# Kernel optimization log

Hardware: AMD Instinct MI355X
Metric: run time of the kernel (lower is better)

## Reference

```python
import jax, jax.numpy as jnp
from jax import lax
import numpy as np
import math

EPS = 1e-5
LEVELS = 17  # quantized levels round(x*255/16) for x in [0,1) -> 0..16


def _bn(x, g, b):
    # training-mode BatchNorm2d: batch statistics over (B,H,W), biased var
    m = x.mean(axis=(0, 2, 3), keepdims=True)
    v = x.var(axis=(0, 2, 3), keepdims=True)
    return (x - m) / jnp.sqrt(v + EPS) * g[None, :, None, None] + b[None, :, None, None]


def _mode_pool_11(x):
    # x is pre-quantized to k*16/256, k in 0..16 -> sliding-window mode via per-level counts
    q = jnp.round(x * 16.0).astype(jnp.int32)  # recover integer level k
    qp = jnp.pad(q, ((0, 0), (0, 0), (5, 5), (5, 5)), mode='reflect')
    oh = (qp[:, :, None, :, :] == jnp.arange(LEVELS, dtype=jnp.int32)[None, None, :, None, None]).astype(jnp.float32)  # [B,C,L,H+10,W+10]
    counts = lax.reduce_window(oh, 0.0, lax.add, (1, 1, 1, 11, 11), (1, 1, 1, 1, 1), 'VALID')  # [B,C,L,H,W]
    lvl = jnp.argmax(counts, axis=2)  # ties -> smallest level, matching torch.mode
    return lvl.astype(x.dtype) * (16.0 / 256.0)


def setup_inputs() -> dict:
    key = jax.random.key(0)
    ks = jax.random.split(key, 8)
    B, C, H, W, F = 2, 3, 512, 512, 16
    x = jax.random.uniform(ks[0], (B, C, H, W), jnp.float32)
    w1 = jax.random.normal(ks[1], (F, C), jnp.float32) * 0.1
    b1 = jnp.zeros((F,), jnp.float32)
    g1 = jnp.ones((F,), jnp.float32); be1 = jnp.zeros((F,), jnp.float32)
    w2 = jax.random.normal(ks[2], (F, F), jnp.float32) * 0.1
    b2 = jnp.zeros((F,), jnp.float32)
    g2 = jnp.ones((F,), jnp.float32); be2 = jnp.zeros((F,), jnp.float32)
    dw = jax.random.normal(ks[3], (F, 1, 3, 3), jnp.float32) * 0.1  # depthwise 3x3
    gd = jnp.ones((F,), jnp.float32); bd = jnp.zeros((F,), jnp.float32)
    ww = jax.random.normal(ks[4], (F,), jnp.float32) * 0.1  # depthwise 1x1 = per-channel scale
    gw = jnp.ones((F,), jnp.float32); bw = jnp.zeros((F,), jnp.float32)
    wh = jax.random.normal(ks[5], (F,), jnp.float32) * 0.1
    gh = jnp.ones((F,), jnp.float32); bh = jnp.zeros((F,), jnp.float32)
    return dict(x=x, w1=w1, b1=b1, g1=g1, be1=be1, w2=w2, b2=b2, g2=g2, be2=be2,
                dw=dw, gd=gd, bd=bd, ww=ww, gw=gw, bw=bw, wh=wh, gh=gh, bh=bh)


def reference(x, w1, b1, g1, be1, w2, b2, g2, be2, dw, gd, bd, ww, gw, bw, wh, gh, bh):
    lrelu = jax.nn.leaky_relu  # default slope 0.01 matches torch LeakyReLU
    x = jnp.round(x * 255.0 / 16.0) * 16.0 / 256.0  # quantize to 16-ish levels
    x = _mode_pool_11(x)
    B, C, H, W = x.shape
    F = w1.shape[0]
    # prepare: two 1x1 conv + BN + LeakyReLU blocks
    p = jnp.einsum('oc,bchw->bohw', w1, x) + b1[None, :, None, None]
    p = lrelu(_bn(p, g1, be1))
    p = jnp.einsum('oc,bchw->bohw', w2, p) + b2[None, :, None, None]
    p = lrelu(_bn(p, g2, be2))
    inter = jnp.stack([p, p], axis=0).reshape(B, 2 * F, H, W)  # mirrors torch stack(dim=0).reshape
    d = p
    n = math.floor(math.log(min(H, W), 3))
    for _ in range(n):
        d = lax.conv_general_dilated(d, dw, (1, 1), 'SAME', feature_group_count=F,
                                     dimension_numbers=('NCHW', 'OIHW', 'NCHW'))
        d = lrelu(_bn(d, gd, bd))
        wdt = lrelu(_bn(d * ww[None, :, None, None], gw, bw))
        hgt = lrelu(_bn(d * wh[None, :, None, None], gh, bh))
        sc = jnp.stack([wdt, hgt], axis=1).reshape(B, 2 * F, H, W)
        inter = sc + inter
    return inter
```

## Files before the change

### kernel.cpp

```cpp
#include <hip/hip_runtime.h>
#include <hip/hip_bf16.h>
#include <stdint.h>
#include <stddef.h>

#define HW 262144
#define EPSF 1e-5f

typedef __hip_bfloat16 bf16;

__device__ __forceinline__ float us2f(uint32_t u){
  union { uint32_t i; float f; } c; c.i = u << 16; return c.f;
}
__device__ __forceinline__ ushort f2bu(float v){
  union { bf16 h; ushort u; } c; c.h = __float2bfloat16(v); return c.u;
}
__device__ __forceinline__ float lrelu(float v){ return v > 0.0f ? v : 0.01f * v; }
__device__ __forceinline__ uint32_t umax2(uint32_t a, uint32_t b){ return a > b ? a : b; }

__global__ __launch_bounds__(256) void k_quant_pad(const float* __restrict__ x,
                                                   uint8_t* __restrict__ qpad){
  int idx = blockIdx.x * 256 + threadIdx.x;
  if (idx >= 6 * 522 * 522) return;
  int pw = idx % 522; int t = idx / 522; int ph = t % 522; int img = t / 522;
  int h = ph - 5; h = h < 0 ? -h : h; if (h > 511) h = 1022 - h;
  int w = pw - 5; w = w < 0 ? -w : w; if (w > 511) w = 1022 - w;
  float v = x[img * HW + h * 512 + w];
  int k = (int)rintf((v * 255.0f) / 16.0f);
  qpad[img * (522 * 528) + ph * 528 + pw] = (uint8_t)k;
}

__global__ __launch_bounds__(256) void k_mode(const uint8_t* __restrict__ qpad,
                                              uint8_t* __restrict__ xm){
  __shared__ uint8_t tile[14 * 528];
  int tid = threadIdx.x;
  int img = blockIdx.x >> 7;
  int h0  = (blockIdx.x & 127) << 2;
  {
    const uint4* g4 = (const uint4*)(qpad + img * (522 * 528) + h0 * 528);
    uint4* t4 = (uint4*)tile;
    t4[tid] = g4[tid];
    if (tid < 206) t4[tid + 256] = g4[tid + 256];
  }
  __syncthreads();
  int r4 = tid >> 6;
  int w0 = (tid & 63) << 3;
  const uint8_t* base = tile + r4 * 528 + w0;
  uint32_t c0 = 0, c1 = 0, c2 = 0, c3 = 0, c4 = 0;
#define HINC(q) { uint32_t inc_ = 1u << (((q) & 3u) << 3); uint32_t rr_ = (q) >> 2; \
    c0 += (rr_==0u)?inc_:0u; c1 += (rr_==1u)?inc_:0u; c2 += (rr_==2u)?inc_:0u; \
    c3 += (rr_==3u)?inc_:0u; c4 += (rr_==4u)?inc_:0u; }
#define HDEC(q) { uint32_t inc_ = 1u << (((q) & 3u) << 3); uint32_t rr_ = (q) >> 2; \
    c0 -= (rr_==0u)?inc_:0u; c1 -= (rr_==1u)?inc_:0u; c2 -= (rr_==2u)?inc_:0u; \
    c3 -= (rr_==3u)?inc_:0u; c4 -= (rr_==4u)?inc_:0u; }
  #pragma unroll 1
  for (int r = 0; r < 11; ++r){
    const uint8_t* row = base + r * 528;
    #pragma unroll
    for (int j = 0; j < 11; ++j){ uint32_t q = row[j]; HINC(q); }
  }
  uint64_t packed = 0;
  #pragma unroll 1
  for (int s = 0; s < 8; ++s){
#define KEY(reg, sh, l) (((((reg) >> (sh)) & 0xffu) << 5) | (16u - (uint32_t)(l)))
    uint32_t m0 = umax2(umax2(KEY(c0,0,0),  KEY(c0,8,1)),  umax2(KEY(c0,16,2),  KEY(c0,24,3)));
    uint32_t m1 = umax2(umax2(KEY(c1,0,4),  KEY(c1,8,5)),  umax2(KEY(c1,16,6),  KEY(c1,24,7)));
    uint32_t m2 = umax2(umax2(KEY(c2,0,8),  KEY(c2,8,9)),  umax2(KEY(c2,16,10), KEY(c2,24,11)));
    uint32_t m3 = umax2(umax2(KEY(c3,0,12), KEY(c3,8,13)), umax2(KEY(c3,16,14), KEY(c3,24,15)));
    uint32_t m  = umax2(umax2(umax2(m0, m1), umax2(m2, m3)), KEY(c4,0,16));
#undef KEY
    uint32_t lvl = 16u - (m & 31u);
    packed |= ((uint64_t)lvl) << (8 * s);
    if (s < 7){
      #pragma unroll
      for (int r = 0; r < 11; ++r){
        uint32_t qo = base[r * 528 + s];      HDEC(qo);
        uint32_t qn = base[r * 528 + s + 11]; HINC(qn);
      }
    }
  }
#undef HINC
#undef HDEC
  *(uint64_t*)(xm + img * HW + (h0 + r4) * 512 + w0) = packed;
}

__device__ __forceinline__ void reduce16(float* su, float* sq, float* __restrict__ partials){
  __shared__ float lsum[32];
  int tid = threadIdx.x;
  if (tid < 32) lsum[tid] = 0.0f;
  __syncthreads();
  #pragma unroll
  for (int o = 0; o < 16; ++o){
    float s = su[o], q = sq[o];
    #pragma unroll
    for (int off = 32; off >= 1; off >>= 1){
      s += __shfl_xor(s, off);
      q += __shfl_xor(q, off);
    }
    if ((tid & 63) == 0){ atomicAdd(&lsum[o], s); atomicAdd(&lsum[16 + o], q); }
  }
  __syncthreads();
  if (tid < 32) partials[blockIdx.x * 32 + tid] = lsum[tid];
}

__global__ __launch_bounds__(256) void k_stats1(const uint8_t* __restrict__ xm,
                                                const float* __restrict__ w1,
                                                const float* __restrict__ b1,
                                                float* __restrict__ partials){
  int t0 = (blockIdx.x * 256 + threadIdx.x) << 2;
  int b = t0 >> 18, hw = t0 & (HW - 1);
  uint32_t q0 = *(const uint32_t*)(xm + (b * 3 + 0) * HW + hw);
  uint32_t q1 = *(const uint32_t*)(xm + (b * 3 + 1) * HW + hw);
  uint32_t q2 = *(const uint32_t*)(xm + (b * 3 + 2) * HW + hw);
  float su[16], sq[16];
  #pragma unroll
  for (int o = 0; o < 16; ++o){ su[o] = 0.0f; sq[o] = 0.0f; }
  #pragma unroll
  for (int px = 0; px < 4; ++px){
    float x0 = (float)((q0 >> (8 * px)) & 0xffu) * 0.0625f;
    float x1 = (float)((q1 >> (8 * px)) & 0xffu) * 0.0625f;
    float x2 = (float)((q2 >> (8 * px)) & 0xffu) * 0.0625f;
    #pragma unroll
    for (int o = 0; o < 16; ++o){
      float v = b1[o] + w1[o*3]*x0 + w1[o*3+1]*x1 + w1[o*3+2]*x2;
      su[o] += v; sq[o] += v * v;
    }
  }
  reduce16(su, sq, partials);
}

__global__ __launch_bounds__(256) void k_stats2(const uint8_t* __restrict__ xm,
                                                const float* __restrict__ w1,
                                                const float* __restrict__ b1,
                                                const float* __restrict__ w2,
                                                const float* __restrict__ b2,
                                                const float* __restrict__ params,
                                                float* __restrict__ partials){
  int t0 = (blockIdx.x * 256 + threadIdx.x) << 2;
  int b = t0 >> 18, hw = t0 & (HW - 1);
  uint32_t q0 = *(const uint32_t*)(xm + (b * 3 + 0) * HW + hw);
  uint32_t q1 = *(const uint32_t*)(xm + (b * 3 + 1) * HW + hw);
  uint32_t q2 = *(const uint32_t*)(xm + (b * 3 + 2) * HW + hw);
  float tv[4][16];
  #pragma unroll
  for (int px = 0; px < 4; ++px){
    float x0 = (float)((q0 >> (8 * px)) & 0xffu) * 0.0625f;
    float x1 = (float)((q1 >> (8 * px)) & 0xffu) * 0.0625f;
    float x2 = (float)((q2 >> (8 * px)) & 0xffu) * 0.0625f;
    #pragma unroll
    for (int o = 0; o < 16; ++o){
      float v = b1[o] + w1[o*3]*x0 + w1[o*3+1]*x1 + w1[o*3+2]*x2;
      tv[px][o] = lrelu(v * params[o] + params[16 + o]);
    }
  }
  float su[16], sq[16];
  #pragma unroll
  for (int o = 0; o < 16; ++o){ su[o] = 0.0f; sq[o] = 0.0f; }
  #pragma unroll
  for (int o = 0; o < 16; ++o){
    #pragma unroll
    for (int px = 0; px < 4; ++px){
      float acc = b2[o];
      #pragma unroll
      for (int c = 0; c < 16; ++c) acc = fmaf(w2[o*16 + c], tv[px][c], acc);
      su[o] += acc; sq[o] += acc * acc;
    }
  }
  reduce16(su, sq, partials);
}

__global__ __launch_bounds__(256) void k_prep(const uint8_t* __restrict__ xm,
                                              const float* __restrict__ w1,
                                              const float* __restrict__ b1,
                                              const float* __restrict__ w2,
                                              const float* __restrict__ b2,
                                              const float* __restrict__ params,
                                              bf16* __restrict__ p){
  int t0 = (blockIdx.x * 256 + threadIdx.x) << 2;
  int b = t0 >> 18, hw = t0 & (HW - 1);
  uint32_t q0 = *(const uint32_t*)(xm + (b * 3 + 0) * HW + hw);
  uint32_t q1 = *(const uint32_t*)(xm + (b * 3 + 1) * HW + hw);
  uint32_t q2 = *(const uint32_t*)(xm + (b * 3 + 2) * HW + hw);
  float tv[4][16];
  #pragma unroll
  for (int px = 0; px < 4; ++px){
    float x0 = (float)((q0 >> (8 * px)) & 0xffu) * 0.0625f;
    float x1 = (float)((q1 >> (8 * px)) & 0xffu) * 0.0625f;
    float x2 = (float)((q2 >> (8 * px)) & 0xffu) * 0.0625f;
    #pragma unroll
    for (int o = 0; o < 16; ++o){
      float v = b1[o] + w1[o*3]*x0 + w1[o*3+1]*x1 + w1[o*3+2]*x2;
      tv[px][o] = lrelu(v * params[o] + params[16 + o]);
    }
  }
  #pragma unroll
  for (int o = 0; o < 16; ++o){
    uint32_t w01 = 0, w23 = 0;
    #pragma unroll
    for (int px = 0; px < 4; ++px){
      float acc = b2[o];
      #pragma unroll
      for (int c = 0; c < 16; ++c) acc = fmaf(w2[o*16 + c], tv[px][c], acc);
      float v = lrelu(acc * params[32 + o] + params[48 + o]);
      uint32_t bits = (uint32_t)f2bu(v);
      if (px == 0) w01 = bits;
      else if (px == 1) w01 |= bits << 16;
      else if (px == 2) w23 = bits;
      else w23 |= bits << 16;
    }
    uint2 ov; ov.x = w01; ov.y = w23;
    *(uint2*)((ushort*)p + (b * 16 + o) * HW + hw) = ov;
  }
}

__device__ __forceinline__ void load_row10(const ushort* __restrict__ rp, int w0, float* v){
  uint4 cc = *(const uint4*)(rp + w0);
  uint32_t l = (w0 == 0)   ? 0u : (uint32_t)rp[w0 - 1];
  uint32_t r = (w0 == 504) ? 0u : (uint32_t)rp[w0 + 8];
  v[0] = us2f(l);
  v[1] = us2f(cc.x & 0xffffu); v[2] = us2f(cc.x >> 16);
  v[3] = us2f(cc.y & 0xffffu); v[4] = us2f(cc.y >> 16);
  v[5] = us2f(cc.z & 0xffffu); v[6] = us2f(cc.z >> 16);
  v[7] = us2f(cc.w & 0xffffu); v[8] = us2f(cc.w >> 16);
  v[9] = us2f(r);
}

__device__ __forceinline__ void zero_row10(float* v){
  #pragma unroll
  for (int j = 0; j < 10; ++j) v[j] = 0.0f;
}

__device__ __forceinline__ void reduce2(float s, float q, float* __restrict__ partials){
  __shared__ float l2[2];
  int tid = threadIdx.x;
  if (tid < 2) l2[tid] = 0.0f;
  __syncthreads();
  #pragma unroll
  for (int off = 32; off >= 1; off >>= 1){
    s += __shfl_xor(s, off);
    q += __shfl_xor(q, off);
  }
  if ((tid & 63) == 0){ atomicAdd(&l2[0], s); atomicAdd(&l2[1], q); }
  __syncthreads();
  if (tid < 2) partials[blockIdx.x * 2 + tid] = l2[tid];
}

__global__ __launch_bounds__(256) void k_convstat(const bf16* __restrict__ d,
                                                  const float* __restrict__ dw,
                                                  float* __restrict__ P1,
                                                  bf16* __restrict__ cout){
  int bid = blockIdx.x;
  int plane = bid >> 7, rg = bid & 127;
  int f = plane & 15;
  int tid = threadIdx.x;
  int h  = (rg << 2) + (tid >> 6);
  int w0 = (tid & 63) << 3;
  const ushort* pl = (const ushort*)d + plane * HW;
  float wf[9];
  #pragma unroll
  for (int i = 0; i < 9; ++i) wf[i] = dw[f * 9 + i];
  float v[3][10];
  #pragma unroll
  for (int dy = 0; dy < 3; ++dy){
    int row = h + dy - 1;
    if ((unsigned)row < 512u) load_row10(pl + row * 512, w0, v[dy]);
    else zero_row10(v[dy]);
  }
  float s = 0.0f, q = 0.0f;
  uint32_t cb[4];
  #pragma unroll
  for (int k = 0; k < 8; ++k){
    float acc = 0.0f;
    #pragma unroll
    for (int dy = 0; dy < 3; ++dy)
      #pragma unroll
      for (int dx = 0; dx < 3; ++dx)
        acc = fmaf(wf[dy*3 + dx], v[dy][k + dx], acc);
    s += acc; q += acc * acc;
    uint32_t bits = (uint32_t)f2bu(acc);
    if ((k & 1) == 0) cb[k >> 1] = bits; else cb[k >> 1] |= bits << 16;
  }
  uint4 cv; cv.x = cb[0]; cv.y = cb[1]; cv.z = cb[2]; cv.w = cb[3];
  *(uint4*)((ushort*)cout + plane * HW + h * 512 + w0) = cv;
  reduce2(s, q, P1);
}

__device__ __forceinline__ void chan_sum_wave(const float* __restrict__ P, int f, int lane,
                                              double& S, double& Q){
  S = 0.0; Q = 0.0;
  #pragma unroll
  for (int i = 0; i < 4; ++i){
    int e = lane + i * 64;
    int blk = (((e >> 7) * 16 + f) << 7) + (e & 127);
    S += (double)P[blk * 2];
    Q += (double)P[blk * 2 + 1];
  }
  #pragma unroll
  for (int off = 32; off >= 1; off >>= 1){
    S += __shfl_xor(S, off);
    Q += __shfl_xor(Q, off);
  }
}

__global__ __launch_bounds__(256) void k_bnfused(const bf16* __restrict__ cin,
                                                 const float* __restrict__ dw,
                                                 const float* __restrict__ gd,
                                                 const float* __restrict__ bd,
                                                 const float* __restrict__ P1in,
                                                 bf16* __restrict__ dout,
                                                 bf16* __restrict__ cout,
                                                 float* __restrict__ P2out,
                                                 float* __restrict__ P1out,
                                                 int write_c){
  __shared__ ushort strip[6][512];
  __shared__ float acc4[4];
  int bid = blockIdx.x;
  int plane = bid >> 7, rg = bid & 127;
  int f = plane & 15;
  int tid = threadIdx.x;

  double S, Q;
  chan_sum_wave(P1in, f, tid & 63, S, Q);
  float sc, sh;
  {
    double m = S / 524288.0;
    double v = Q / 524288.0 - m * m;
    sc = gd[f] / sqrtf((float)v + EPSF);
    sh = bd[f] - (float)m * sc;
  }
  if (tid < 4) acc4[tid] = 0.0f;

  int h0 = rg << 2;
  int h  = h0 + (tid >> 6);
  int w0 = (tid & 63) << 3;
  const ushort* cpl = (const ushort*)cin + plane * HW;

  float s2 = 0.0f, q2 = 0.0f;
  {
    uint4 cv = *(const uint4*)(cpl + h * 512 + w0);
    float cf[8];
    cf[0] = us2f(cv.x & 0xffffu); cf[1] = us2f(cv.x >> 16);
    cf[2] = us2f(cv.y & 0xffffu); cf[3] = us2f(cv.y >> 16);
    cf[4] = us2f(cv.z & 0xffffu); cf[5] = us2f(cv.z >> 16);
    cf[6] = us2f(cv.w & 0xffffu); cf[7] = us2f(cv.w >> 16);
    uint32_t ob[4];
    #pragma unroll
    for (int k = 0; k < 8; ++k){
      float vv = lrelu(fmaf(cf[k], sc, sh));
      uint32_t bits = (uint32_t)f2bu(vv);
      if ((k & 1) == 0) ob[k >> 1] = bits; else ob[k >> 1] |= bits << 16;
      s2 += vv; q2 += vv * vv;
    }
    uint4 ov; ov.x = ob[0]; ov.y = ob[1]; ov.z = ob[2]; ov.w = ob[3];
    *(uint4*)((ushort*)dout + plane * HW + h * 512 + w0) = ov;
    *(uint4*)&strip[1 + (tid >> 6)][w0] = ov;
  }

  if (tid < 128){
    int hh = (tid < 64) ? (h0 - 1) : (h0 + 4);
    int si = (tid < 64) ? 0 : 5;
    int wh0 = (tid & 63) << 3;
    uint4 hv; hv.x = 0; hv.y = 0; hv.z = 0; hv.w = 0;
    if ((unsigned)hh < 512u){
      uint4 cv = *(const uint4*)(cpl + hh * 512 + wh0);
      float cf[8];
      cf[0] = us2f(cv.x & 0xffffu); cf[1] = us2f(cv.x >> 16);
      cf[2] = us2f(cv.y & 0xffffu); cf[3] = us2f(cv.y >> 16);
      cf[4] = us2f(cv.z & 0xffffu); cf[5] = us2f(cv.z >> 16);
      cf[6] = us2f(cv.w & 0xffffu); cf[7] = us2f(cv.w >> 16);
      uint32_t hb[4];
      #pragma unroll
      for (int k = 0; k < 8; ++k){
        float vv = lrelu(fmaf(cf[k], sc, sh));
        uint32_t bits = (uint32_t)f2bu(vv);
        if ((k & 1) == 0) hb[k >> 1] = bits; else hb[k >> 1] |= bits << 16;
      }
      hv.x = hb[0]; hv.y = hb[1]; hv.z = hb[2]; hv.w = hb[3];
    }
    *(uint4*)&strip[si][wh0] = hv;
  }
  __syncthreads();

  float wf[9];
  #pragma unroll
  for (int i = 0; i < 9; ++i) wf[i] = dw[f * 9 + i];
  float s1 = 0.0f, q1 = 0.0f;
  {
    int si = 1 + (tid >> 6);
    float v[3][10];
    #pragma unroll
    for (int dy = 0; dy < 3; ++dy)
      load_row10(&strip[si - 1 + dy][0], w0, v[dy]);
    uint32_t cb[4];
    #pragma unroll
    for (int k = 0; k < 8; ++k){
      float acc = 0.0f;
      #pragma unroll
      for (int dy = 0; dy < 3; ++dy)
        #pragma unroll
        for (int dx = 0; dx < 3; ++dx)
          acc = fmaf(wf[dy*3 + dx], v[dy][k + dx], acc);
      s1 += acc; q1 += acc * acc;
      uint32_t bits = (uint32_t)f2bu(acc);
      if ((k & 1) == 0) cb[k >> 1] = bits; else cb[k >> 1] |= bits << 16;
    }
    if (write_c){
      uint4 cv2; cv2.x = cb[0]; cv2.y = cb[1]; cv2.z = cb[2]; cv2.w = cb[3];
      *(uint4*)((ushort*)cout + plane * HW + h * 512 + w0) = cv2;
    }
  }

  #pragma unroll
  for (int off = 32; off >= 1; off >>= 1){
    s2 += __shfl_xor(s2, off);
    q2 += __shfl_xor(q2, off);
    s1 += __shfl_xor(s1, off);
    q1 += __shfl_xor(q1, off);
  }
  if ((tid & 63) == 0){
    atomicAdd(&acc4[0], s2); atomicAdd(&acc4[1], q2);
    atomicAdd(&acc4[2], s1); atomicAdd(&acc4[3], q1);
  }
  __syncthreads();
  if (tid < 2)      P2out[bid * 2 + tid]       = acc4[tid];
  else if (tid < 4) P1out[bid * 2 + (tid - 2)] = acc4[tid];
}

__global__ __launch_bounds__(256) void k_fin_prep(const float* __restrict__ partials,
                                                  const float* __restrict__ g,
                                                  const float* __restrict__ bb,
                                                  float* __restrict__ params,
                                                  int offS, int offT){
  int tid = threadIdx.x;
  int o = tid & 15, c = tid >> 4;
  double S = 0.0, Q = 0.0;
  for (int i = c * 32; i < (c + 1) * 32; ++i){
    S += (double)partials[i * 32 + o];
    Q += (double)partials[i * 32 + 16 + o];
  }
  __shared__ double lS[256], lQ[256];
  lS[tid] = S; lQ[tid] = Q; __syncthreads();
  for (int st = 8; st >= 1; st >>= 1){
    if (c < st){ lS[tid] += lS[tid + st * 16]; lQ[tid] += lQ[tid + st * 16]; }
    __syncthreads();
  }
  if (tid < 16){
    double m = lS[tid] / 524288.0;
    double v = lQ[tid] / 524288.0 - m * m;
    float sc = g[tid] / sqrtf((float)v + EPSF);
    params[offS + tid] = sc;
    params[offT + tid] = bb[tid] - (float)m * sc;
  }
}

__global__ __launch_bounds__(256) void k_fin_all(const float* __restrict__ P2,
                                                 const float* __restrict__ ww,
                                                 const float* __restrict__ gw,
                                                 const float* __restrict__ bw,
                                                 const float* __restrict__ wh,
                                                 const float* __restrict__ gh,
                                                 const float* __restrict__ bh,
                                                 float* __restrict__ dparams){
  int tid = threadIdx.x;
  int wid = tid >> 6, lane = tid & 63;
  int pair = blockIdx.x * 4 + wid;
  int t = pair >> 4, f = pair & 15;
  double S, Q;
  chan_sum_wave(P2 + t * 8192, f, lane, S, Q);
  if (lane == 0){
    float m = (float)(S / 524288.0);
    float v = (float)(Q / 524288.0) - m * m;
    float sw = ww[f] * gw[f] / sqrtf(ww[f] * ww[f] * v + EPSF);
    float tw = bw[f] - m * sw;
    float s2 = wh[f] * gh[f] / sqrtf(wh[f] * wh[f] * v + EPSF);
    float t2 = bh[f] - m * s2;
    dparams[t * 64 + f]      = sw;
    dparams[t * 64 + 16 + f] = tw;
    dparams[t * 64 + 32 + f] = s2;
    dparams[t * 64 + 48 + f] = t2;
  }
}

__device__ __forceinline__ void conv8(uint4 cc, float* v){
  v[0] = us2f(cc.x & 0xffffu); v[1] = us2f(cc.x >> 16);
  v[2] = us2f(cc.y & 0xffffu); v[3] = us2f(cc.y >> 16);
  v[4] = us2f(cc.z & 0xffffu); v[5] = us2f(cc.z >> 16);
  v[6] = us2f(cc.w & 0xffffu); v[7] = us2f(cc.w >> 16);
}

__global__ __launch_bounds__(256) void k_final(const bf16* __restrict__ p,
                                               const bf16* __restrict__ d1,
                                               const bf16* __restrict__ d2,
                                               const bf16* __restrict__ d3,
                                               const bf16* __restrict__ d4,
                                               const bf16* __restrict__ d5,
                                               const float* __restrict__ dparams,
                                               float* __restrict__ out){
  int tid = threadIdx.x;
  int f = blockIdx.x >> 7;
  int gid = blockIdx.x * 256 + tid;
  int hw = (gid & 32767) << 3;
  int fo = f * HW + hw;
  int f1 = (16 + f) * HW + hw;

  uint4 rp0 = *(const uint4*)((const ushort*)p + fo);
  uint4 rp1 = *(const uint4*)((const ushort*)p + f1);
  uint4 r0a = *(const uint4*)((const ushort*)d1 + fo);
  uint4 r0b = *(const uint4*)((const ushort*)d1 + f1);
  uint4 r1a = *(const uint4*)((const ushort*)d2 + fo);
  uint4 r1b = *(const uint4*)((const ushort*)d2 + f1);
  uint4 r2a = *(const uint4*)((const ushort*)d3 + fo);
  uint4 r2b = *(const uint4*)((const ushort*)d3 + f1);
  uint4 r3a = *(const uint4*)((const ushort*)d4 + fo);
  uint4 r3b = *(const uint4*)((const ushort*)d4 + f1);
  uint4 r4a = *(const uint4*)((const ushort*)d5 + fo);
  uint4 r4b = *(const uint4*)((const ushort*)d5 + f1);

  float swA[5], twA[5], shA[5], thA[5];
  #pragma unroll
  for (int t = 0; t < 5; ++t){
    swA[t] = dparams[t * 64 + f];
    twA[t] = dparams[t * 64 + 16 + f];
    shA[t] = dparams[t * 64 + 32 + f];
    thA[t] = dparams[t * 64 + 48 + f];
  }

  float pf[8], pg[8];
  conv8(rp0, pf); conv8(rp1, pg);
  float a00[8], a01[8], a10[8], a11[8];
  #pragma unroll
  for (int k = 0; k < 8; ++k){ a00[k] = pf[k]; a01[k] = pg[k]; a10[k] = pf[k]; a11[k] = pg[k]; }

  uint4 ra[5] = { r0a, r1a, r2a, r3a, r4a };
  uint4 rb[5] = { r0b, r1b, r2b, r3b, r4b };
  #pragma unroll
  for (int t = 0; t < 5; ++t){
    float dv0[8], dv1[8];
    conv8(ra[t], dv0); conv8(rb[t], dv1);
    float sw = swA[t], tw = twA[t], sh = shA[t], th = thA[t];
    #pragma unroll
    for (int k = 0; k < 8; ++k){
      a00[k] += lrelu(fmaf(dv0[k], sw, tw));
      a01[k] += lrelu(fmaf(dv0[k], sh, th));
      a10[k] += lrelu(fmaf(dv1[k], sw, tw));
      a11[k] += lrelu(fmaf(dv1[k], sh, th));
    }
  }
  #pragma unroll
  for (int half = 0; half < 2; ++half){
    float4 v0 = { a00[half*4+0], a00[half*4+1], a00[half*4+2], a00[half*4+3] };
    float4 v1 = { a01[half*4+0], a01[half*4+1], a01[half*4+2], a01[half*4+3] };
    float4 v2 = { a10[half*4+0], a10[half*4+1], a10[half*4+2], a10[half*4+3] };
    float4 v3 = { a11[half*4+0], a11[half*4+1], a11[half*4+2], a11[half*4+3] };
    *(float4*)(out + f * HW + hw + half*4)        = v0;
    *(float4*)(out + (16 + f) * HW + hw + half*4) = v1;
    *(float4*)(out + (32 + f) * HW + hw + half*4) = v2;
    *(float4*)(out + (48 + f) * HW + hw + half*4) = v3;
  }
}

extern "C" void kernel_launch(void* const* d_in, const int* in_sizes, int n_in,
                              void* d_out, int out_size, void* d_ws, size_t ws_size,
                              hipStream_t stream){
  (void)in_sizes; (void)n_in; (void)out_size;
  const float* x   = (const float*)d_in[0];
  const float* w1  = (const float*)d_in[1];
  const float* b1  = (const float*)d_in[2];
  const float* g1  = (const float*)d_in[3];
  const float* be1 = (const float*)d_in[4];
  const float* w2  = (const float*)d_in[5];
  const float* b2  = (const float*)d_in[6];
  const float* g2  = (const float*)d_in[7];
  const float* be2 = (const float*)d_in[8];
  const float* dw  = (const float*)d_in[9];
  const float* gd  = (const float*)d_in[10];
  const float* bd  = (const float*)d_in[11];
  const float* ww  = (const float*)d_in[12];
  const float* gw  = (const float*)d_in[13];
  const float* bw  = (const float*)d_in[14];
  const float* wh  = (const float*)d_in[15];
  const float* gh  = (const float*)d_in[16];
  const float* bh  = (const float*)d_in[17];
  float* out = (float*)d_out;

  char* ws = (char*)d_ws;
  size_t off = 0;
  auto alloc = [&](size_t sz) -> void* {
    void* ptr = ws + off;
    off = (off + sz + 4095) & ~(size_t)4095;
    return ptr;
  };
  uint8_t* qpad  = (uint8_t*)alloc((size_t)6 * 522 * 528);
  uint8_t* xm    = (uint8_t*)alloc((size_t)6 * HW);
  bf16*    p     = (bf16*)   alloc((size_t)32 * HW * 2);
  bf16*    dbuf[5];
  for (int i = 0; i < 5; ++i) dbuf[i] = (bf16*)alloc((size_t)32 * HW * 2);
  float*   Pp     = (float*)  alloc((size_t)512 * 32 * 4);
  float*   P1a    = (float*)  alloc((size_t)4096 * 2 * 4);
  float*   P1b    = (float*)  alloc((size_t)4096 * 2 * 4);
  float*   P2     = (float*)  alloc((size_t)5 * 4096 * 2 * 4);
  float*   params = (float*)  alloc(4096);
  float*   dparams= (float*)  alloc(4096);
  if (ws_size < off) return;

  bf16* cbuf_a = (bf16*)(out + 8 * 1024 * 1024);
  bf16* cbuf_b = cbuf_a + (size_t)32 * HW;

  k_quant_pad<<<dim3((6*522*522 + 255)/256), dim3(256), 0, stream>>>(x, qpad);
  k_mode     <<<dim3(768), dim3(256), 0, stream>>>(qpad, xm);
  k_stats1   <<<dim3(512), dim3(256), 0, stream>>>(xm, w1, b1, Pp);
  k_fin_prep <<<dim3(1),   dim3(256), 0, stream>>>(Pp, g1, be1, params, 0, 16);
  k_stats2   <<<dim3(512), dim3(256), 0, stream>>>(xm, w1, b1, w2, b2, params, Pp);
  k_fin_prep <<<dim3(1),   dim3(256), 0, stream>>>(Pp, g2, be2, params, 32, 48);
  k_prep     <<<dim3(512), dim3(256), 0, stream>>>(xm, w1, b1, w2, b2, params, p);
  k_convstat <<<dim3(4096), dim3(256), 0, stream>>>(p, dw, P1a, cbuf_a);

  bf16* cin = cbuf_a; bf16* cout = cbuf_b;
  float* Pin = P1a; float* Pout = P1b;
  for (int t = 0; t < 5; ++t){
    k_bnfused<<<dim3(4096), dim3(256), 0, stream>>>(cin, dw, gd, bd, Pin,
                                                    dbuf[t], cout, P2 + t * 8192,
                                                    Pout, (t < 4) ? 1 : 0);
    bf16* ctmp = cin; cin = cout; cout = ctmp;
    float* tmp = Pin; Pin = Pout; Pout = tmp;
  }
  k_fin_all<<<dim3(20), dim3(256), 0, stream>>>(P2, ww, gw, bw, wh, gh, bh, dparams);
  k_final<<<dim3(2048), dim3(256), 0, stream>>>(p, dbuf[0], dbuf[1], dbuf[2],
                                                dbuf[3], dbuf[4], dparams, out);
}
```

Measured before the change: 223.6 us.

## Fuse conv loop, stats finalize and output into one persistent kernel with grid barriers

Replaces the separate convstat, five bnfused launches, fin_all and final kernels with a single 1024-block persistent kernel. Device-wide atomic-counter barriers separate the iterations, and each block now processes 16 rows instead of 4. The aim is to remove roughly eight kernel launches and their gaps, and to cut halo re-reads. It depends on all 1024 blocks being co-resident, which launch_bounds(256,4) is meant to allow on the device's CUs. If they are not co-resident the barrier can deadlock, and each barrier adds spin-wait cost.

```diff
diff --git a/kernel.cpp b/kernel.cpp
--- a/kernel.cpp
+++ b/kernel.cpp
@@ -5,6 +5,7 @@
 
 #define HW 262144
 #define EPSF 1e-5f
+#define NBLK 1024
 
 typedef __hip_bfloat16 bf16;
 
@@ -174,7 +175,9 @@
                                               const float* __restrict__ w2,
                                               const float* __restrict__ b2,
                                               const float* __restrict__ params,
-                                              bf16* __restrict__ p){
+                                              bf16* __restrict__ p,
+                                              unsigned* __restrict__ barcnt){
+  if (blockIdx.x == 0 && threadIdx.x == 0) *barcnt = 0u;
   int t0 = (blockIdx.x * 256 + threadIdx.x) << 2;
   int b = t0 >> 18, hw = t0 & (HW - 1);
   uint32_t q0 = *(const uint32_t*)(xm + (b * 3 + 0) * HW + hw);
@@ -210,219 +213,6 @@
     uint2 ov; ov.x = w01; ov.y = w23;
     *(uint2*)((ushort*)p + (b * 16 + o) * HW + hw) = ov;
   }
-}
-
-__device__ __forceinline__ void load_row10(const ushort* __restrict__ rp, int w0, float* v){
-  uint4 cc = *(const uint4*)(rp + w0);
-  uint32_t l = (w0 == 0)   ? 0u : (uint32_t)rp[w0 - 1];
-  uint32_t r = (w0 == 504) ? 0u : (uint32_t)rp[w0 + 8];
-  v[0] = us2f(l);
-  v[1] = us2f(cc.x & 0xffffu); v[2] = us2f(cc.x >> 16);
-  v[3] = us2f(cc.y & 0xffffu); v[4] = us2f(cc.y >> 16);
-  v[5] = us2f(cc.z & 0xffffu); v[6] = us2f(cc.z >> 16);
-  v[7] = us2f(cc.w & 0xffffu); v[8] = us2f(cc.w >> 16);
-  v[9] = us2f(r);
-}
-
-__device__ __forceinline__ void zero_row10(float* v){
-  #pragma unroll
-  for (int j = 0; j < 10; ++j) v[j] = 0.0f;
-}
-
-__device__ __forceinline__ void reduce2(float s, float q, float* __restrict__ partials){
-  __shared__ float l2[2];
-  int tid = threadIdx.x;
-  if (tid < 2) l2[tid] = 0.0f;
-  __syncthreads();
-  #pragma unroll
-  for (int off = 32; off >= 1; off >>= 1){
-    s += __shfl_xor(s, off);
-    q += __shfl_xor(q, off);
-  }
-  if ((tid & 63) == 0){ atomicAdd(&l2[0], s); atomicAdd(&l2[1], q); }
-  __syncthreads();
-  if (tid < 2) partials[blockIdx.x * 2 + tid] = l2[tid];
-}
-
-__global__ __launch_bounds__(256) void k_convstat(const bf16* __restrict__ d,
-                                                  const float* __restrict__ dw,
-                                                  float* __restrict__ P1,
-                                                  bf16* __restrict__ cout){
-  int bid = blockIdx.x;
-  int plane = bid >> 7, rg = bid & 127;
-  int f = plane & 15;
-  int tid = threadIdx.x;
-  int h  = (rg << 2) + (tid >> 6);
-  int w0 = (tid & 63) << 3;
-  const ushort* pl = (const ushort*)d + plane * HW;
-  float wf[9];
-  #pragma unroll
-  for (int i = 0; i < 9; ++i) wf[i] = dw[f * 9 + i];
-  float v[3][10];
-  #pragma unroll
-  for (int dy = 0; dy < 3; ++dy){
-    int row = h + dy - 1;
-    if ((unsigned)row < 512u) load_row10(pl + row * 512, w0, v[dy]);
-    else zero_row10(v[dy]);
-  }
-  float s = 0.0f, q = 0.0f;
-  uint32_t cb[4];
-  #pragma unroll
-  for (int k = 0; k < 8; ++k){
-    float acc = 0.0f;
-    #pragma unroll
-    for (int dy = 0; dy < 3; ++dy)
-      #pragma unroll
-      for (int dx = 0; dx < 3; ++dx)
-        acc = fmaf(wf[dy*3 + dx], v[dy][k + dx], acc);
-    s += acc; q += acc * acc;
-    uint32_t bits = (uint32_t)f2bu(acc);
-    if ((k & 1) == 0) cb[k >> 1] = bits; else cb[k >> 1] |= bits << 16;
-  }
-  uint4 cv; cv.x = cb[0]; cv.y = cb[1]; cv.z = cb[2]; cv.w = cb[3];
-  *(uint4*)((ushort*)cout + plane * HW + h * 512 + w0) = cv;
-  reduce2(s, q, P1);
-}
-
-__device__ __forceinline__ void chan_sum_wave(const float* __restrict__ P, int f, int lane,
-                                              double& S, double& Q){
-  S = 0.0; Q = 0.0;
-  #pragma unroll
-  for (int i = 0; i < 4; ++i){
-    int e = lane + i * 64;
-    int blk = (((e >> 7) * 16 + f) << 7) + (e & 127);
-    S += (double)P[blk * 2];
-    Q += (double)P[blk * 2 + 1];
-  }
-  #pragma unroll
-  for (int off = 32; off >= 1; off >>= 1){
-    S += __shfl_xor(S, off);
-    Q += __shfl_xor(Q, off);
-  }
-}
-
-__global__ __launch_bounds__(256) void k_bnfused(const bf16* __restrict__ cin,
-                                                 const float* __restrict__ dw,
-                                                 const float* __restrict__ gd,
-                                                 const float* __restrict__ bd,
-                                                 const float* __restrict__ P1in,
-                                                 bf16* __restrict__ dout,
-                                                 bf16* __restrict__ cout,
-                                                 float* __restrict__ P2out,
-                                                 float* __restrict__ P1out,
-                                                 int write_c){
-  __shared__ ushort strip[6][512];
-  __shared__ float acc4[4];
-  int bid = blockIdx.x;
-  int plane = bid >> 7, rg = bid & 127;
-  int f = plane & 15;
-  int tid = threadIdx.x;
-
-  double S, Q;
-  chan_sum_wave(P1in, f, tid & 63, S, Q);
-  float sc, sh;
-  {
-    double m = S / 524288.0;
-    double v = Q / 524288.0 - m * m;
-    sc = gd[f] / sqrtf((float)v + EPSF);
-    sh = bd[f] - (float)m * sc;
-  }
-  if (tid < 4) acc4[tid] = 0.0f;
-
-  int h0 = rg << 2;
-  int h  = h0 + (tid >> 6);
-  int w0 = (tid & 63) << 3;
-  const ushort* cpl = (const ushort*)cin + plane * HW;
-
-  float s2 = 0.0f, q2 = 0.0f;
-  {
-    uint4 cv = *(const uint4*)(cpl + h * 512 + w0);
-    float cf[8];
-    cf[0] = us2f(cv.x & 0xffffu); cf[1] = us2f(cv.x >> 16);
-    cf[2] = us2f(cv.y & 0xffffu); cf[3] = us2f(cv.y >> 16);
-    cf[4] = us2f(cv.z & 0xffffu); cf[5] = us2f(cv.z >> 16);
-    cf[6] = us2f(cv.w & 0xffffu); cf[7] = us2f(cv.w >> 16);
-    uint32_t ob[4];
-    #pragma unroll
-    for (int k = 0; k < 8; ++k){
-      float vv = lrelu(fmaf(cf[k], sc, sh));
-      uint32_t bits = (uint32_t)f2bu(vv);
-      if ((k & 1) == 0) ob[k >> 1] = bits; else ob[k >> 1] |= bits << 16;
-      s2 += vv; q2 += vv * vv;
-    }
-    uint4 ov; ov.x = ob[0]; ov.y = ob[1]; ov.z = ob[2]; ov.w = ob[3];
-    *(uint4*)((ushort*)dout + plane * HW + h * 512 + w0) = ov;
-    *(uint4*)&strip[1 + (tid >> 6)][w0] = ov;
-  }
-
-  if (tid < 128){
-    int hh = (tid < 64) ? (h0 - 1) : (h0 + 4);
-    int si = (tid < 64) ? 0 : 5;
-    int wh0 = (tid & 63) << 3;
-    uint4 hv; hv.x = 0; hv.y = 0; hv.z = 0; hv.w = 0;
-    if ((unsigned)hh < 512u){
-      uint4 cv = *(const uint4*)(cpl + hh * 512 + wh0);
-      float cf[8];
-      cf[0] = us2f(cv.x & 0xffffu); cf[1] = us2f(cv.x >> 16);
-      cf[2] = us2f(cv.y & 0xffffu); cf[3] = us2f(cv.y >> 16);
-      cf[4] = us2f(cv.z & 0xffffu); cf[5] = us2f(cv.z >> 16);
-      cf[6] = us2f(cv.w & 0xffffu); cf[7] = us2f(cv.w >> 16);
-      uint32_t hb[4];
-      #pragma unroll
-      for (int k = 0; k < 8; ++k){
-        float vv = lrelu(fmaf(cf[k], sc, sh));
-        uint32_t bits = (uint32_t)f2bu(vv);
-        if ((k & 1) == 0) hb[k >> 1] = bits; else hb[k >> 1] |= bits << 16;
-      }
-      hv.x = hb[0]; hv.y = hb[1]; hv.z = hb[2]; hv.w = hb[3];
-    }
-    *(uint4*)&strip[si][wh0] = hv;
-  }
-  __syncthreads();
-
-  float wf[9];
-  #pragma unroll
-  for (int i = 0; i < 9; ++i) wf[i] = dw[f * 9 + i];
-  float s1 = 0.0f, q1 = 0.0f;
-  {
-    int si = 1 + (tid >> 6);
-    float v[3][10];
-    #pragma unroll
-    for (int dy = 0; dy < 3; ++dy)
-      load_row10(&strip[si - 1 + dy][0], w0, v[dy]);
-    uint32_t cb[4];
-    #pragma unroll
-    for (int k = 0; k < 8; ++k){
-      float acc = 0.0f;
-      #pragma unroll
-      for (int dy = 0; dy < 3; ++dy)
-        #pragma unroll
-        for (int dx = 0; dx < 3; ++dx)
-          acc = fmaf(wf[dy*3 + dx], v[dy][k + dx], acc);
-      s1 += acc; q1 += acc * acc;
-      uint32_t bits = (uint32_t)f2bu(acc);
-      if ((k & 1) == 0) cb[k >> 1] = bits; else cb[k >> 1] |= bits << 16;
-    }
-    if (write_c){
-      uint4 cv2; cv2.x = cb[0]; cv2.y = cb[1]; cv2.z = cb[2]; cv2.w = cb[3];
-      *(uint4*)((ushort*)cout + plane * HW + h * 512 + w0) = cv2;
-    }
-  }
-
-  #pragma unroll
-  for (int off = 32; off >= 1; off >>= 1){
-    s2 += __shfl_xor(s2, off);
-    q2 += __shfl_xor(q2, off);
-    s1 += __shfl_xor(s1, off);
-    q1 += __shfl_xor(q1, off);
-  }
-  if ((tid & 63) == 0){
-    atomicAdd(&acc4[0], s2); atomicAdd(&acc4[1], q2);
-    atomicAdd(&acc4[2], s1); atomicAdd(&acc4[3], q1);
-  }
-  __syncthreads();
-  if (tid < 2)      P2out[bid * 2 + tid]       = acc4[tid];
-  else if (tid < 4) P1out[bid * 2 + (tid - 2)] = acc4[tid];
 }
 
 __global__ __launch_bounds__(256) void k_fin_prep(const float* __restrict__ partials,
@@ -452,109 +242,289 @@
   }
 }
 
-__global__ __launch_bounds__(256) void k_fin_all(const float* __restrict__ P2,
-                                                 const float* __restrict__ ww,
-                                                 const float* __restrict__ gw,
-                                                 const float* __restrict__ bw,
-                                                 const float* __restrict__ wh,
-                                                 const float* __restrict__ gh,
-                                                 const float* __restrict__ bh,
-                                                 float* __restrict__ dparams){
+__device__ __forceinline__ void load_row10(const ushort* __restrict__ rp, int w0, float* v){
+  uint4 cc = *(const uint4*)(rp + w0);
+  uint32_t l = (w0 == 0)   ? 0u : (uint32_t)rp[w0 - 1];
+  uint32_t r = (w0 == 504) ? 0u : (uint32_t)rp[w0 + 8];
+  v[0] = us2f(l);
+  v[1] = us2f(cc.x & 0xffffu); v[2] = us2f(cc.x >> 16);
+  v[3] = us2f(cc.y & 0xffffu); v[4] = us2f(cc.y >> 16);
+  v[5] = us2f(cc.z & 0xffffu); v[6] = us2f(cc.z >> 16);
+  v[7] = us2f(cc.w & 0xffffu); v[8] = us2f(cc.w >> 16);
+  v[9] = us2f(r);
+}
+
+__device__ __forceinline__ void chan_sum64(const float* __restrict__ P, int f, int lane,
+                                           double& S, double& Q){
+  int b = lane >> 5, rgx = lane & 31;
+  int blk = ((b * 16 + f) << 5) + rgx;
+  S = (double)P[blk * 2];
+  Q = (double)P[blk * 2 + 1];
+  #pragma unroll
+  for (int off = 32; off >= 1; off >>= 1){
+    S += __shfl_xor(S, off);
+    Q += __shfl_xor(Q, off);
+  }
+}
+
+__device__ __forceinline__ void gbar(unsigned* cnt, unsigned target){
+  __syncthreads();
+  if (threadIdx.x == 0){
+    __threadfence();
+    atomicAdd(cnt, 1u);
+    while (atomicAdd(cnt, 0u) < target) __builtin_amdgcn_s_sleep(8);
+    __threadfence();
+  }
+  __syncthreads();
+}
+
+__global__ __launch_bounds__(256, 4) void k_loop(
+    const bf16* __restrict__ p, const float* __restrict__ dw,
+    const float* __restrict__ gd, const float* __restrict__ bd,
+    bf16* __restrict__ cbuf_a, bf16* __restrict__ cbuf_b,
+    bf16* d0, bf16* d1, bf16* d2, bf16* d3, bf16* d4,
+    float* __restrict__ P1a, float* __restrict__ P1b, float* __restrict__ P2,
+    const float* __restrict__ ww, const float* __restrict__ gw,
+    const float* __restrict__ bw, const float* __restrict__ wh,
+    const float* __restrict__ gh, const float* __restrict__ bh,
+    float* __restrict__ out, unsigned* __restrict__ barcnt){
+  __shared__ ushort strip[18][512];
+  __shared__ float acc4[4];
+  __shared__ float sparams[20];
+  __shared__ bf16* sdbuf[5];
+  int bid = blockIdx.x;
   int tid = threadIdx.x;
-  int wid = tid >> 6, lane = tid & 63;
-  int pair = blockIdx.x * 4 + wid;
-  int t = pair >> 4, f = pair & 15;
-  double S, Q;
-  chan_sum_wave(P2 + t * 8192, f, lane, S, Q);
-  if (lane == 0){
-    float m = (float)(S / 524288.0);
-    float v = (float)(Q / 524288.0) - m * m;
-    float sw = ww[f] * gw[f] / sqrtf(ww[f] * ww[f] * v + EPSF);
-    float tw = bw[f] - m * sw;
-    float s2 = wh[f] * gh[f] / sqrtf(wh[f] * wh[f] * v + EPSF);
-    float t2 = bh[f] - m * s2;
-    dparams[t * 64 + f]      = sw;
-    dparams[t * 64 + 16 + f] = tw;
-    dparams[t * 64 + 32 + f] = s2;
-    dparams[t * 64 + 48 + f] = t2;
-  }
-}
-
-__device__ __forceinline__ void conv8(uint4 cc, float* v){
-  v[0] = us2f(cc.x & 0xffffu); v[1] = us2f(cc.x >> 16);
-  v[2] = us2f(cc.y & 0xffffu); v[3] = us2f(cc.y >> 16);
-  v[4] = us2f(cc.z & 0xffffu); v[5] = us2f(cc.z >> 16);
-  v[6] = us2f(cc.w & 0xffffu); v[7] = us2f(cc.w >> 16);
-}
-
-__global__ __launch_bounds__(256) void k_final(const bf16* __restrict__ p,
-                                               const bf16* __restrict__ d1,
-                                               const bf16* __restrict__ d2,
-                                               const bf16* __restrict__ d3,
-                                               const bf16* __restrict__ d4,
-                                               const bf16* __restrict__ d5,
-                                               const float* __restrict__ dparams,
-                                               float* __restrict__ out){
-  int tid = threadIdx.x;
-  int f = blockIdx.x >> 7;
-  int gid = blockIdx.x * 256 + tid;
-  int hw = (gid & 32767) << 3;
-  int fo = f * HW + hw;
-  int f1 = (16 + f) * HW + hw;
-
-  uint4 rp0 = *(const uint4*)((const ushort*)p + fo);
-  uint4 rp1 = *(const uint4*)((const ushort*)p + f1);
-  uint4 r0a = *(const uint4*)((const ushort*)d1 + fo);
-  uint4 r0b = *(const uint4*)((const ushort*)d1 + f1);
-  uint4 r1a = *(const uint4*)((const ushort*)d2 + fo);
-  uint4 r1b = *(const uint4*)((const ushort*)d2 + f1);
-  uint4 r2a = *(const uint4*)((const ushort*)d3 + fo);
-  uint4 r2b = *(const uint4*)((const ushort*)d3 + f1);
-  uint4 r3a = *(const uint4*)((const ushort*)d4 + fo);
-  uint4 r3b = *(const uint4*)((const ushort*)d4 + f1);
-  uint4 r4a = *(const uint4*)((const ushort*)d5 + fo);
-  uint4 r4b = *(const uint4*)((const ushort*)d5 + f1);
-
-  float swA[5], twA[5], shA[5], thA[5];
-  #pragma unroll
+  int plane = bid >> 5, rg = bid & 31;
+  int f = plane & 15;
+  int h0 = rg << 4;
+  int w0 = (tid & 63) << 3;
+  int sr0 = tid >> 6;
+  if (tid == 0){ sdbuf[0]=d0; sdbuf[1]=d1; sdbuf[2]=d2; sdbuf[3]=d3; sdbuf[4]=d4; }
+  if (tid < 4) acc4[tid] = 0.0f;
+  float wf[9];
+  #pragma unroll
+  for (int i = 0; i < 9; ++i) wf[i] = dw[f * 9 + i];
+
+  {
+    const ushort* pl = (const ushort*)p + plane * HW;
+    #pragma unroll
+    for (int rr = 0; rr < 4; ++rr){
+      int row = h0 + rr * 4 + sr0;
+      uint4 v = *(const uint4*)(pl + row * 512 + w0);
+      *(uint4*)&strip[1 + rr * 4 + sr0][w0] = v;
+    }
+    if (tid < 128){
+      int hh = (tid < 64) ? h0 - 1 : h0 + 16;
+      int si = (tid < 64) ? 0 : 17;
+      int wh0 = (tid & 63) << 3;
+      uint4 v; v.x = 0; v.y = 0; v.z = 0; v.w = 0;
+      if ((unsigned)hh < 512u) v = *(const uint4*)(pl + hh * 512 + wh0);
+      *(uint4*)&strip[si][wh0] = v;
+    }
+    __syncthreads();
+    float s1 = 0.0f, q1 = 0.0f;
+    ushort* ca = (ushort*)cbuf_a + plane * HW;
+    #pragma unroll
+    for (int rr = 0; rr < 4; ++rr){
+      int sr = 1 + rr * 4 + sr0;
+      float v[3][10];
+      #pragma unroll
+      for (int dy = 0; dy < 3; ++dy) load_row10(&strip[sr - 1 + dy][0], w0, v[dy]);
+      uint32_t cb[4];
+      #pragma unroll
+      for (int k = 0; k < 8; ++k){
+        float acc = 0.0f;
+        #pragma unroll
+        for (int dy = 0; dy < 3; ++dy)
+          #pragma unroll
+          for (int dx = 0; dx < 3; ++dx)
+            acc = fmaf(wf[dy*3 + dx], v[dy][k + dx], acc);
+        s1 += acc; q1 += acc * acc;
+        uint32_t bits = (uint32_t)f2bu(acc);
+        if ((k & 1) == 0) cb[k >> 1] = bits; else cb[k >> 1] |= bits << 16;
+      }
+      uint4 cv; cv.x = cb[0]; cv.y = cb[1]; cv.z = cb[2]; cv.w = cb[3];
+      *(uint4*)(ca + (h0 + rr * 4 + sr0) * 512 + w0) = cv;
+    }
+    #pragma unroll
+    for (int off = 32; off >= 1; off >>= 1){
+      s1 += __shfl_xor(s1, off); q1 += __shfl_xor(q1, off);
+    }
+    if ((tid & 63) == 0){ atomicAdd(&acc4[0], s1); atomicAdd(&acc4[1], q1); }
+    __syncthreads();
+    if (tid < 2) P1a[bid * 2 + tid] = acc4[tid];
+  }
+  gbar(barcnt, 1 * NBLK);
+
+  bf16* cin = cbuf_a; bf16* cot = cbuf_b;
+  float* Pin = P1a; float* Pout = P1b;
+  #pragma unroll 1
   for (int t = 0; t < 5; ++t){
-    swA[t] = dparams[t * 64 + f];
-    twA[t] = dparams[t * 64 + 16 + f];
-    shA[t] = dparams[t * 64 + 32 + f];
-    thA[t] = dparams[t * 64 + 48 + f];
-  }
-
-  float pf[8], pg[8];
-  conv8(rp0, pf); conv8(rp1, pg);
-  float a00[8], a01[8], a10[8], a11[8];
-  #pragma unroll
-  for (int k = 0; k < 8; ++k){ a00[k] = pf[k]; a01[k] = pg[k]; a10[k] = pf[k]; a11[k] = pg[k]; }
-
-  uint4 ra[5] = { r0a, r1a, r2a, r3a, r4a };
-  uint4 rb[5] = { r0b, r1b, r2b, r3b, r4b };
-  #pragma unroll
-  for (int t = 0; t < 5; ++t){
-    float dv0[8], dv1[8];
-    conv8(ra[t], dv0); conv8(rb[t], dv1);
-    float sw = swA[t], tw = twA[t], sh = shA[t], th = thA[t];
-    #pragma unroll
-    for (int k = 0; k < 8; ++k){
-      a00[k] += lrelu(fmaf(dv0[k], sw, tw));
-      a01[k] += lrelu(fmaf(dv0[k], sh, th));
-      a10[k] += lrelu(fmaf(dv1[k], sw, tw));
-      a11[k] += lrelu(fmaf(dv1[k], sh, th));
-    }
-  }
-  #pragma unroll
-  for (int half = 0; half < 2; ++half){
-    float4 v0 = { a00[half*4+0], a00[half*4+1], a00[half*4+2], a00[half*4+3] };
-    float4 v1 = { a01[half*4+0], a01[half*4+1], a01[half*4+2], a01[half*4+3] };
-    float4 v2 = { a10[half*4+0], a10[half*4+1], a10[half*4+2], a10[half*4+3] };
-    float4 v3 = { a11[half*4+0], a11[half*4+1], a11[half*4+2], a11[half*4+3] };
-    *(float4*)(out + f * HW + hw + half*4)        = v0;
-    *(float4*)(out + (16 + f) * HW + hw + half*4) = v1;
-    *(float4*)(out + (32 + f) * HW + hw + half*4) = v2;
-    *(float4*)(out + (48 + f) * HW + hw + half*4) = v3;
+    double S, Q;
+    chan_sum64(Pin, f, tid & 63, S, Q);
+    float sc, sh;
+    { double m = S / 524288.0;
+      double vv = Q / 524288.0 - m * m;
+      sc = gd[f] / sqrtf((float)vv + EPSF);
+      sh = bd[f] - (float)m * sc; }
+    if (tid < 4) acc4[tid] = 0.0f;
+    const ushort* cpl = (const ushort*)cin + plane * HW;
+    ushort* dpl = (ushort*)sdbuf[t] + plane * HW;
+    float s2 = 0.0f, q2 = 0.0f;
+    #pragma unroll
+    for (int rr = 0; rr < 4; ++rr){
+      int row = h0 + rr * 4 + sr0;
+      uint4 cv = *(const uint4*)(cpl + row * 512 + w0);
+      float cf[8];
+      cf[0] = us2f(cv.x & 0xffffu); cf[1] = us2f(cv.x >> 16);
+      cf[2] = us2f(cv.y & 0xffffu); cf[3] = us2f(cv.y >> 16);
+      cf[4] = us2f(cv.z & 0xffffu); cf[5] = us2f(cv.z >> 16);
+      cf[6] = us2f(cv.w & 0xffffu); cf[7] = us2f(cv.w >> 16);
+      uint32_t ob[4];
+      #pragma unroll
+      for (int k = 0; k < 8; ++k){
+        float vv = lrelu(fmaf(cf[k], sc, sh));
+        uint32_t bits = (uint32_t)f2bu(vv);
+        if ((k & 1) == 0) ob[k >> 1] = bits; else ob[k >> 1] |= bits << 16;
+        s2 += vv; q2 += vv * vv;
+      }
+      uint4 ov; ov.x = ob[0]; ov.y = ob[1]; ov.z = ob[2]; ov.w = ob[3];
+      *(uint4*)(dpl + row * 512 + w0) = ov;
+      *(uint4*)&strip[1 + rr * 4 + sr0][w0] = ov;
+    }
+    if (tid < 128){
+      int hh = (tid < 64) ? h0 - 1 : h0 + 16;
+      int si = (tid < 64) ? 0 : 17;
+      int wh0 = (tid & 63) << 3;
+      uint4 hv; hv.x = 0; hv.y = 0; hv.z = 0; hv.w = 0;
+      if ((unsigned)hh < 512u){
+        uint4 cv = *(const uint4*)(cpl + hh * 512 + wh0);
+        float cf[8];
+        cf[0] = us2f(cv.x & 0xffffu); cf[1] = us2f(cv.x >> 16);
+        cf[2] = us2f(cv.y & 0xffffu); cf[3] = us2f(cv.y >> 16);
+        cf[4] = us2f(cv.z & 0xffffu); cf[5] = us2f(cv.z >> 16);
+        cf[6] = us2f(cv.w & 0xffffu); cf[7] = us2f(cv.w >> 16);
+        uint32_t hb[4];
+        #pragma unroll
+        for (int k = 0; k < 8; ++k){
+          float vv = lrelu(fmaf(cf[k], sc, sh));
+          uint32_t bits = (uint32_t)f2bu(vv);
+          if ((k & 1) == 0) hb[k >> 1] = bits; else hb[k >> 1] |= bits << 16;
+        }
+        hv.x = hb[0]; hv.y = hb[1]; hv.z = hb[2]; hv.w = hb[3];
+      }
+      *(uint4*)&strip[si][wh0] = hv;
+    }
+    __syncthreads();
+    float s1 = 0.0f, q1 = 0.0f;
+    ushort* co = (ushort*)cot + plane * HW;
+    #pragma unroll
+    for (int rr = 0; rr < 4; ++rr){
+      int sr = 1 + rr * 4 + sr0;
+      float v[3][10];
+      #pragma unroll
+      for (int dy = 0; dy < 3; ++dy) load_row10(&strip[sr - 1 + dy][0], w0, v[dy]);
+      uint32_t cb[4];
+      #pragma unroll
+      for (int k = 0; k < 8; ++k){
+        float acc = 0.0f;
+        #pragma unroll
+        for (int dy = 0; dy < 3; ++dy)
+          #pragma unroll
+          for (int dx = 0; dx < 3; ++dx)
+            acc = fmaf(wf[dy*3 + dx], v[dy][k + dx], acc);
+        s1 += acc; q1 += acc * acc;
+        uint32_t bits = (uint32_t)f2bu(acc);
+        if ((k & 1) == 0) cb[k >> 1] = bits; else cb[k >> 1] |= bits << 16;
+      }
+      if (t < 4){
+        uint4 cv2; cv2.x = cb[0]; cv2.y = cb[1]; cv2.z = cb[2]; cv2.w = cb[3];
+        *(uint4*)(co + (h0 + rr * 4 + sr0) * 512 + w0) = cv2;
+      }
+    }
+    #pragma unroll
+    for (int off = 32; off >= 1; off >>= 1){
+      s2 += __shfl_xor(s2, off); q2 += __shfl_xor(q2, off);
+      s1 += __shfl_xor(s1, off); q1 += __shfl_xor(q1, off);
+    }
+    if ((tid & 63) == 0){
+      atomicAdd(&acc4[0], s2); atomicAdd(&acc4[1], q2);
+      atomicAdd(&acc4[2], s1); atomicAdd(&acc4[3], q1);
+    }
+    __syncthreads();
+    if (tid < 2)      P2[t * 2048 + bid * 2 + tid] = acc4[tid];
+    else if (tid < 4) Pout[bid * 2 + (tid - 2)]    = acc4[tid];
+    gbar(barcnt, (unsigned)(2 + t) * NBLK);
+    { bf16* tm = cin; cin = cot; cot = tm; }
+    { float* tp = Pin; Pin = Pout; Pout = tp; }
+  }
+
+  {
+    int ff = bid >> 6;
+    int sub = bid & 63;
+    int wid = tid >> 6, lane = tid & 63;
+    for (int t = wid; t < 5; t += 4){
+      double S, Q;
+      chan_sum64(P2 + t * 2048, ff, lane, S, Q);
+      if (lane == 0){
+        float m = (float)(S / 524288.0);
+        float vv = (float)(Q / 524288.0) - m * m;
+        float sw = ww[ff] * gw[ff] / sqrtf(ww[ff] * ww[ff] * vv + EPSF);
+        float tw = bw[ff] - m * sw;
+        float s2p = wh[ff] * gh[ff] / sqrtf(wh[ff] * wh[ff] * vv + EPSF);
+        float t2p = bh[ff] - m * s2p;
+        sparams[t * 4 + 0] = sw; sparams[t * 4 + 1] = tw;
+        sparams[t * 4 + 2] = s2p; sparams[t * 4 + 3] = t2p;
+      }
+    }
+    __syncthreads();
+    #pragma unroll 1
+    for (int ch = 0; ch < 2; ++ch){
+      int hw = sub * 4096 + tid * 16 + ch * 8;
+      int fo = ff * HW + hw;
+      int f1 = (16 + ff) * HW + hw;
+      uint4 rp0 = *(const uint4*)((const ushort*)p + fo);
+      uint4 rp1 = *(const uint4*)((const ushort*)p + f1);
+      float pf[8], pg[8];
+      pf[0]=us2f(rp0.x&0xffffu); pf[1]=us2f(rp0.x>>16); pf[2]=us2f(rp0.y&0xffffu); pf[3]=us2f(rp0.y>>16);
+      pf[4]=us2f(rp0.z&0xffffu); pf[5]=us2f(rp0.z>>16); pf[6]=us2f(rp0.w&0xffffu); pf[7]=us2f(rp0.w>>16);
+      pg[0]=us2f(rp1.x&0xffffu); pg[1]=us2f(rp1.x>>16); pg[2]=us2f(rp1.y&0xffffu); pg[3]=us2f(rp1.y>>16);
+      pg[4]=us2f(rp1.z&0xffffu); pg[5]=us2f(rp1.z>>16); pg[6]=us2f(rp1.w&0xffffu); pg[7]=us2f(rp1.w>>16);
+      float a00[8], a01[8], a10[8], a11[8];
+      #pragma unroll
+      for (int k = 0; k < 8; ++k){ a00[k]=pf[k]; a01[k]=pg[k]; a10[k]=pf[k]; a11[k]=pg[k]; }
+      #pragma unroll
+      for (int t = 0; t < 5; ++t){
+        const ushort* dp = (const ushort*)sdbuf[t];
+        uint4 ra = *(const uint4*)(dp + fo);
+        uint4 rb = *(const uint4*)(dp + f1);
+        float dv0[8], dv1[8];
+        dv0[0]=us2f(ra.x&0xffffu); dv0[1]=us2f(ra.x>>16); dv0[2]=us2f(ra.y&0xffffu); dv0[3]=us2f(ra.y>>16);
+        dv0[4]=us2f(ra.z&0xffffu); dv0[5]=us2f(ra.z>>16); dv0[6]=us2f(ra.w&0xffffu); dv0[7]=us2f(ra.w>>16);
+        dv1[0]=us2f(rb.x&0xffffu); dv1[1]=us2f(rb.x>>16); dv1[2]=us2f(rb.y&0xffffu); dv1[3]=us2f(rb.y>>16);
+        dv1[4]=us2f(rb.z&0xffffu); dv1[5]=us2f(rb.z>>16); dv1[6]=us2f(rb.w&0xffffu); dv1[7]=us2f(rb.w>>16);
+        float sw = sparams[t*4+0], tw = sparams[t*4+1];
+        float sh2 = sparams[t*4+2], th = sparams[t*4+3];
+        #pragma unroll
+        for (int k = 0; k < 8; ++k){
+          a00[k] += lrelu(fmaf(dv0[k], sw, tw));
+          a01[k] += lrelu(fmaf(dv0[k], sh2, th));
+          a10[k] += lrelu(fmaf(dv1[k], sw, tw));
+          a11[k] += lrelu(fmaf(dv1[k], sh2, th));
+        }
+      }
+      #pragma unroll
+      for (int half = 0; half < 2; ++half){
+        float4 v0 = { a00[half*4+0], a00[half*4+1], a00[half*4+2], a00[half*4+3] };
+        float4 v1 = { a01[half*4+0], a01[half*4+1], a01[half*4+2], a01[half*4+3] };
+        float4 v2 = { a10[half*4+0], a10[half*4+1], a10[half*4+2], a10[half*4+3] };
+        float4 v3 = { a11[half*4+0], a11[half*4+1], a11[half*4+2], a11[half*4+3] };
+        *(float4*)(out + ff * HW + hw + half*4)        = v0;
+        *(float4*)(out + (16 + ff) * HW + hw + half*4) = v1;
+        *(float4*)(out + (32 + ff) * HW + hw + half*4) = v2;
+        *(float4*)(out + (48 + ff) * HW + hw + half*4) = v3;
+      }
+    }
   }
 }
 
@@ -595,11 +565,11 @@
   bf16*    dbuf[5];
   for (int i = 0; i < 5; ++i) dbuf[i] = (bf16*)alloc((size_t)32 * HW * 2);
   float*   Pp     = (float*)  alloc((size_t)512 * 32 * 4);
-  float*   P1a    = (float*)  alloc((size_t)4096 * 2 * 4);
-  float*   P1b    = (float*)  alloc((size_t)4096 * 2 * 4);
-  float*   P2     = (float*)  alloc((size_t)5 * 4096 * 2 * 4);
+  float*   P1a    = (float*)  alloc((size_t)NBLK * 2 * 4);
+  float*   P1b    = (float*)  alloc((size_t)NBLK * 2 * 4);
+  float*   P2     = (float*)  alloc((size_t)5 * NBLK * 2 * 4);
   float*   params = (float*)  alloc(4096);
-  float*   dparams= (float*)  alloc(4096);
+  unsigned* barcnt= (unsigned*)alloc(4096);
   if (ws_size < off) return;
 
   bf16* cbuf_a = (bf16*)(out + 8 * 1024 * 1024);
@@ -611,19 +581,9 @@
   k_fin_prep <<<dim3(1),   dim3(256), 0, stream>>>(Pp, g1, be1, params, 0, 16);
   k_stats2   <<<dim3(512), dim3(256), 0, stream>>>(xm, w1, b1, w2, b2, params, Pp);
   k_fin_prep <<<dim3(1),   dim3(256), 0, stream>>>(Pp, g2, be2, params, 32, 48);
-  k_prep     <<<dim3(512), dim3(256), 0, stream>>>(xm, w1, b1, w2, b2, params, p);
-  k_convstat <<<dim3(4096), dim3(256), 0, stream>>>(p, dw, P1a, cbuf_a);
-
-  bf16* cin = cbuf_a; bf16* cout = cbuf_b;
-  float* Pin = P1a; float* Pout = P1b;
-  for (int t = 0; t < 5; ++t){
-    k_bnfused<<<dim3(4096), dim3(256), 0, stream>>>(cin, dw, gd, bd, Pin,
-                                                    dbuf[t], cout, P2 + t * 8192,
-                                                    Pout, (t < 4) ? 1 : 0);
-    bf16* ctmp = cin; cin = cout; cout = ctmp;
-    float* tmp = Pin; Pin = Pout; Pout = tmp;
-  }
-  k_fin_all<<<dim3(20), dim3(256), 0, stream>>>(P2, ww, gw, bw, wh, gh, bh, dparams);
-  k_final<<<dim3(2048), dim3(256), 0, stream>>>(p, dbuf[0], dbuf[1], dbuf[2],
-                                                dbuf[3], dbuf[4], dparams, out);
-}
+  k_prep     <<<dim3(512), dim3(256), 0, stream>>>(xm, w1, b1, w2, b2, params, p, barcnt);
+  k_loop     <<<dim3(NBLK), dim3(256), 0, stream>>>(
+      p, dw, gd, bd, cbuf_a, cbuf_b,
+      dbuf[0], dbuf[1], dbuf[2], dbuf[3], dbuf[4],
+      P1a, P1b, P2, ww, gw, bw, wh, gh, bh, out, barcnt);
+}
```

After: 812.4 us. +263.3%, slower.
